# Kernel optimization log

Hardware: AMD Instinct MI355X
Metric: run time of the kernel (lower is better)

Reference implementation:

```python
import jax, jax.numpy as jnp
import numpy as np

B, L, D_IN = 4, 2048, 80
D, H, DFF, WIN = 128, 16, 128, 64
DH = D // H
BN_EPS = 1e-5


def sinusoidal_positional_encoding(l, d, dtype):
    # Faithful to source: pos_j = 10000 ** (j / d) (exponent j/d, not 2j/d)
    n = d // 2 + (d % 2 == 1)
    pos_i = jnp.arange(l, dtype=dtype)[:, None]                  # [L,1]
    pos_j = jnp.power(jnp.asarray(10000.0, dtype), jnp.arange(n, dtype=dtype) / d)  # [n]
    ang = pos_i / pos_j                                          # [L,n]
    pos = jnp.stack([jnp.sin(ang), jnp.cos(ang)], axis=-1).reshape(l, -1)
    return pos[:, :d]                                            # [L,D]


def local_window_disallowed_mask(l, win):
    # Source: mask starts as ones (True = disallowed), zeros only strictly
    i = jnp.arange(l)
    diff = jnp.abs(i[:, None] - i[None, :])
    allowed = (diff >= 1) & (diff <= win)
    return ~allowed                                              # [L,L] bool, True = masked


def setup_inputs() -> dict:
    key = jax.random.key(0)
    ks = jax.random.split(key, 17)
    s = 0.05  # weight scale for numerical stability
    return {
        "x": jax.random.normal(ks[0], (B, L, D_IN), jnp.float32),
        "conv_w": jax.random.normal(ks[1], (D, D_IN), jnp.float32) * s,
        "conv_b": jax.random.normal(ks[2], (D,), jnp.float32) * s,
        "bn_g": jax.random.uniform(ks[3], (D,), jnp.float32, 0.5, 1.5),
        "bn_b": jax.random.normal(ks[4], (D,), jnp.float32) * s,
        "bn_rm": jax.random.normal(ks[5], (D,), jnp.float32) * s,
        "bn_rv": jax.random.uniform(ks[6], (D,), jnp.float32, 0.5, 1.5),
        "in_proj_w": jax.random.normal(ks[7], (3 * D, D), jnp.float32) * s,
        "in_proj_b": jax.random.normal(ks[8], (3 * D,), jnp.float32) * s,
        "out_w": jax.random.normal(ks[9], (D, D), jnp.float32) * s,
        "out_b": jax.random.normal(ks[10], (D,), jnp.float32) * s,
        "ff_w1": jax.random.normal(ks[11], (DFF, D), jnp.float32) * s,
        "ff_b1": jax.random.normal(ks[12], (DFF,), jnp.float32) * s,
        "ff_w2": jax.random.normal(ks[13], (D, DFF), jnp.float32) * s,
        "ff_b2": jax.random.normal(ks[14], (D,), jnp.float32) * s,
        "fc_w": jax.random.normal(ks[15], (D_IN, D), jnp.float32) * s,
        "fc_b": jax.random.normal(ks[16], (D_IN,), jnp.float32) * s,
    }


def _forward(x, conv_w, conv_b, bn_g, bn_b, bn_rm, bn_rv,
             in_proj_w, in_proj_b, out_w, out_b,
             ff_w1, ff_b1, ff_w2, ff_b2, fc_w, fc_b):
    b, l, _ = x.shape
    dt = x.dtype
    # Conv1d(kernel=1) + ReLU + BatchNorm1d (eval mode, running stats)
    h = jax.nn.relu(jnp.einsum('bli,oi->blo', x, conv_w) + conv_b)     # [B,L,D]
    h = (h - bn_rm) * (bn_g * jax.lax.rsqrt(bn_rv + BN_EPS)) + bn_b
    # positional encoding
    h = h + sinusoidal_positional_encoding(l, D, dt)
    # MultiheadAttention (torch semantics: joint in_proj, scaled dot, out_proj)
    qkv = jnp.einsum('bld,ed->ble', h, in_proj_w) + in_proj_b          # [B,L,3D]
    q, k, v = jnp.split(qkv, 3, axis=-1)
    q = q.reshape(b, l, H, DH).transpose(0, 2, 1, 3)                   # [B,H,L,dh]
    k = k.reshape(b, l, H, DH).transpose(0, 2, 1, 3)
    v = v.reshape(b, l, H, DH).transpose(0, 2, 1, 3)
    scores = jnp.einsum('bhqd,bhkd->bhqk', q, k) / jnp.sqrt(jnp.asarray(DH, dt))
    mask = local_window_disallowed_mask(l, WIN)                        # True = masked
    scores = jnp.where(mask, jnp.finfo(dt).min, scores)
    attn = jax.nn.softmax(scores, axis=-1)                             # [B,H,L,L]
    ctx = jnp.einsum('bhqk,bhkd->bhqd', attn, v)
    ctx = ctx.transpose(0, 2, 1, 3).reshape(b, l, D)
    attn_out = jnp.einsum('bld,od->blo', ctx, out_w) + out_b           # [B,L,D]
    # FFN (no residual in source)
    f = jax.nn.relu(jnp.einsum('bld,fd->blf', attn_out, ff_w1) + ff_b1)
    f = jnp.einsum('blf,df->bld', f, ff_w2) + ff_b2                    # [B,L,D]
    # final head
    return jnp.einsum('bld,od->blo', f, fc_w) + fc_b                   # [B,L,80]


def reference(x, conv_w, conv_b, bn_g, bn_b, bn_rm, bn_rv,
              in_proj_w, in_proj_b, out_w, out_b,
              ff_w1, ff_b1, ff_w2, ff_b2, fc_w, fc_b):
    return _forward(x, conv_w, conv_b, bn_g, bn_b, bn_rm, bn_rv,
                    in_proj_w, in_proj_b, out_w, out_b,
                    ff_w1, ff_b1, ff_w2, ff_b2, fc_w, fc_b)
```

## Files before the change

### kernel.cpp

```cpp
#include <hip/hip_runtime.h>
#include <math.h>

constexpr int L_ = 2048, D_ = 128, H_ = 16;
constexpr int T_ = 8192;
constexpr int DIN = 80;
constexpr int LDX = T_;

typedef __attribute__((ext_vector_type(8))) short short8;
typedef __attribute__((ext_vector_type(4))) float floatx4;

__device__ float g_xT  [DIN * T_];
__device__ float g_posT[D_ * L_];
__device__ unsigned short g_h_hi[T_ * D_];
__device__ unsigned short g_h_lo[T_ * D_];
__device__ unsigned short g_Wq_hi[3 * D_ * D_];
__device__ unsigned short g_Wq_lo[3 * D_ * D_];
__device__ float g_qkv [3 * D_ * T_];
__device__ unsigned short g_ctxH[T_ * D_];
__device__ unsigned short g_ctxL[T_ * D_];
__device__ unsigned short g_Mf1H[D_ * D_];
__device__ unsigned short g_Mf1L[D_ * D_];
__device__ unsigned short g_MfcH[D_ * D_];
__device__ unsigned short g_MfcL[D_ * D_];
__device__ float g_WconvT[DIN * D_];
__device__ float g_bf1   [D_];
__device__ float g_bfc   [D_];

__device__ __forceinline__ unsigned short bf16h(float x) {
    unsigned u = __float_as_uint(x);
    return (unsigned short)((u + 0x7FFFu + ((u >> 16) & 1u)) >> 16);
}
__device__ __forceinline__ float bf16f(unsigned short h) {
    return __uint_as_float(((unsigned)h) << 16);
}

__global__ __launch_bounds__(256) void prep_kernel(
        const float* __restrict__ x,
        const float* __restrict__ conv_w,
        const float* __restrict__ in_proj_w,
        const float* __restrict__ out_w,  const float* __restrict__ out_b,
        const float* __restrict__ ff_w1,  const float* __restrict__ ff_b1,
        const float* __restrict__ ff_w2,  const float* __restrict__ ff_b2,
        const float* __restrict__ fc_w,   const float* __restrict__ fc_b) {
    __shared__ float smem[80 * 65];
    int bid = blockIdx.x, tid = threadIdx.x;

    if (bid < 128) {
        int t0 = bid * 64;
        for (int i = tid; i < 64 * 80; i += 256) {
            int t = i / 80, k = i - t * 80;
            smem[k * 65 + t] = x[(size_t)t0 * 80 + i];
        }
        __syncthreads();
        for (int i = tid; i < 80 * 64; i += 256) {
            int k = i >> 6, tt = i & 63;
            g_xT[(size_t)k * T_ + t0 + tt] = smem[k * 65 + tt];
        }
        return;
    }
    if (bid < 640) {
        int idx = (bid - 128) * 256 + tid;
        int l = idx >> 6, j = idx & 63;
        float inv = __expf((float)j * (-9.210340371976184f / 128.0f));
        float ang = (float)l * inv;
        g_posT[(2 * j) * L_ + l]     = sinf(ang);
        g_posT[(2 * j + 1) * L_ + l] = cosf(ang);
        return;
    }
    if (bid < 680) {
        int e = (bid - 640) * 256 + tid;
        int o = e / 80, k = e - o * 80;
        g_WconvT[k * D_ + o] = conv_w[e];
        return;
    }
    if (bid < 872) {
        int e = (bid - 680) * 256 + tid;
        float v = in_proj_w[e];
        unsigned short hi = bf16h(v);
        g_Wq_hi[e] = hi;
        g_Wq_lo[e] = bf16h(v - bf16f(hi));
        return;
    }
    float* rowbuf = smem;
    float* red = smem + 256;
    if (bid < 936) {
        int sub = tid >> 7, k = tid & 127;
        int f = (bid - 872) * 2 + sub;
        rowbuf[sub * 128 + k] = ff_w1[f * 128 + k];
        __syncthreads();
        float acc = 0.f;
#pragma unroll 8
        for (int o = 0; o < 128; o++)
            acc = fmaf(rowbuf[sub * 128 + o], out_w[o * 128 + k], acc);
        unsigned short hi = bf16h(acc);
        g_Mf1H[f * 128 + k] = hi;
        g_Mf1L[f * 128 + k] = bf16h(acc - bf16f(hi));
        red[tid] = rowbuf[sub * 128 + k] * out_b[k];
        __syncthreads();
        for (int s = 64; s > 0; s >>= 1) {
            if (k < s) red[tid] += red[tid + s];
            __syncthreads();
        }
        if (k == 0) g_bf1[f] = red[sub * 128] + ff_b1[f];
        return;
    }
    {
        int sub = tid >> 7, k = tid & 127;
        int o = (bid - 936) * 2 + sub;
        rowbuf[sub * 128 + k] = (o < 80) ? fc_w[o * 128 + k] : 0.f;
        __syncthreads();
        float acc = 0.f;
#pragma unroll 8
        for (int d = 0; d < 128; d++)
            acc = fmaf(rowbuf[sub * 128 + d], ff_w2[d * 128 + k], acc);
        unsigned short hi = bf16h(acc);
        g_MfcH[o * 128 + k] = hi;
        g_MfcL[o * 128 + k] = bf16h(acc - bf16f(hi));
        red[tid] = rowbuf[sub * 128 + k] * ff_b2[k];
        __syncthreads();
        for (int s = 64; s > 0; s >>= 1) {
            if (k < s) red[tid] += red[tid + s];
            __syncthreads();
        }
        if (k == 0) g_bfc[o] = (o < 80) ? (red[sub * 128] + fc_b[o]) : 0.f;
        return;
    }
}

__global__ __launch_bounds__(256) void conv_kernel(
        const float* __restrict__ X, const float* __restrict__ Wt,
        const float* __restrict__ bias,
        const float* __restrict__ bg, const float* __restrict__ bb,
        const float* __restrict__ brm, const float* __restrict__ brv) {
    constexpr int BK = 80, BN = 32, TN = 2;
    __shared__ float Xs[BK][64];
    __shared__ float Ws[BK][BN];
    int tid = threadIdx.x;
    int t0 = blockIdx.x * 64;
    int cb = blockIdx.y * BN;
    int tc = tid & 15, tr = tid >> 4;

    float acc[4][TN] = {};
    for (int i = tid; i < BK * 16; i += 256) {
        int k = i >> 4, f = i & 15;
        *(float4*)&Xs[k][f * 4] =
            *(const float4*)&X[(size_t)k * LDX + t0 + f * 4];
    }
    for (int i = tid; i < BK * (BN / 4); i += 256) {
        int k = i / (BN / 4), f = i - k * (BN / 4);
        *(float4*)&Ws[k][f * 4] =
            *(const float4*)&Wt[(size_t)k * D_ + cb + f * 4];
    }
    __syncthreads();
#pragma unroll 4
    for (int k = 0; k < BK; ++k) {
        float4 a = *(float4*)&Xs[k][tr * 4];
        float av[4] = {a.x, a.y, a.z, a.w};
        float wv[TN];
#pragma unroll
        for (int jj = 0; jj < TN; jj++) wv[jj] = Ws[k][tc * TN + jj];
#pragma unroll
        for (int i = 0; i < 4; i++)
#pragma unroll
            for (int jj = 0; jj < TN; jj++)
                acc[i][jj] = fmaf(av[i], wv[jj], acc[i][jj]);
    }

#pragma unroll
    for (int i = 0; i < 4; i++) {
        int t = t0 + tr * 4 + i;
        unsigned hi2 = 0, lo2 = 0;
#pragma unroll
        for (int jj = 0; jj < TN; jj++) {
            int c = cb + tc * TN + jj;
            float v = acc[i][jj] + bias[c];
            v = fmaxf(v, 0.0f);
            v = (v - brm[c]) * (bg[c] * rsqrtf(brv[c] + 1e-5f)) + bb[c];
            v += g_posT[c * L_ + (t & 2047)];
            unsigned short h = bf16h(v);
            float lo = v - bf16f(h);
            hi2 |= ((unsigned)h) << (16 * jj);
            lo2 |= ((unsigned)bf16h(lo)) << (16 * jj);
        }
        int cbase = cb + tc * TN;
        *(unsigned*)&g_h_hi[(size_t)t * 128 + cbase] = hi2;
        *(unsigned*)&g_h_lo[(size_t)t * 128 + cbase] = lo2;
    }
}

__global__ __launch_bounds__(256) void qkv_mfma(const float* __restrict__ in_proj_b) {
    __shared__ unsigned short WsH[64 * 136];
    __shared__ unsigned short WsL[64 * 136];
    __shared__ unsigned short HsH[32 * 136];
    __shared__ unsigned short HsL[32 * 136];
    int tid = threadIdx.x;
    int t0 = blockIdx.x * 32;
    int cb = blockIdx.y * 64;

    for (int i = tid; i < 1024; i += 256) {
        int r = i >> 4, c8 = (i & 15) * 8;
        *(uint4*)&WsH[r * 136 + c8] = *(const uint4*)&g_Wq_hi[(size_t)(cb + r) * 128 + c8];
        *(uint4*)&WsL[r * 136 + c8] = *(const uint4*)&g_Wq_lo[(size_t)(cb + r) * 128 + c8];
    }
    for (int i = tid; i < 512; i += 256) {
        int r = i >> 4, c8 = (i & 15) * 8;
        *(uint4*)&HsH[r * 136 + c8] = *(const uint4*)&g_h_hi[(size_t)(t0 + r) * 128 + c8];
        *(uint4*)&HsL[r * 136 + c8] = *(const uint4*)&g_h_lo[(size_t)(t0 + r) * 128 + c8];
    }
    __syncthreads();

    int lane = tid & 63, w = tid >> 6;
    int m16 = lane & 15, quad = lane >> 4;
    int c0 = w * 16;

    short8 aH[4], aL[4];
#pragma unroll
    for (int kt = 0; kt < 4; kt++) {
        aH[kt] = *(short8*)&WsH[(c0 + m16) * 136 + kt * 32 + quad * 8];
        aL[kt] = *(short8*)&WsL[(c0 + m16) * 136 + kt * 32 + quad * 8];
    }
    float bias_r[4];
#pragma unroll
    for (int r = 0; r < 4; r++) bias_r[r] = in_proj_b[cb + c0 + quad * 4 + r];

#pragma unroll
    for (int s = 0; s < 2; s++) {
        floatx4 acc = {0.f, 0.f, 0.f, 0.f};
        int trow = s * 16 + m16;
#pragma unroll
        for (int kt = 0; kt < 4; kt++) {
            short8 bH = *(short8*)&HsH[trow * 136 + kt * 32 + quad * 8];
            short8 bL = *(short8*)&HsL[trow * 136 + kt * 32 + quad * 8];
            acc = __builtin_amdgcn_mfma_f32_16x16x32_bf16(aH[kt], bH, acc, 0, 0, 0);
            acc = __builtin_amdgcn_mfma_f32_16x16x32_bf16(aL[kt], bH, acc, 0, 0, 0);
            acc = __builtin_amdgcn_mfma_f32_16x16x32_bf16(aH[kt], bL, acc, 0, 0, 0);
        }
#pragma unroll
        for (int r = 0; r < 4; r++)
            g_qkv[(size_t)(cb + c0 + quad * 4 + r) * LDX + t0 + s * 16 + m16] =
                acc[r] + bias_r[r];
    }
}

__global__ __launch_bounds__(256) void attn_kernel() {
    __shared__ float4 SK[2][2][324];
    __shared__ float4 SV[2][2][324];
    int bh = blockIdx.x;
    int qb = blockIdx.y * 512;
    int b = bh >> 4, h = bh & 15;
    int tb = b * L_;
    int tid = threadIdx.x;
    int jbase = qb - 64;

    for (int c16 = 0; c16 < 16; c16++) {
        int d = c16 & 7;
        int ch = ((c16 < 8) ? D_ : 2 * D_) + h * 8 + d;
        const float* src = g_qkv + (size_t)ch * LDX + tb;
        float4* base4 = ((c16 < 8) ? &SK[0][0][0] : &SV[0][0][0]) + (d >> 2) * 324;
        for (int s = tid; s < 641; s += 256) {
            int j = jbase + s;
            float v = ((unsigned)j < (unsigned)L_) ? src[j] : 0.f;
            ((float*)(base4 + (s & 1) * 648 + (s >> 1)))[d & 3] = v;
        }
    }
    __syncthreads();

    const float sc = 0.35355339059327373f;
    int q0 = qb + 2 * tid;
    float qa[8], qc[8];
#pragma unroll
    for (int d = 0; d < 8; d++) {
        qa[d] = g_qkv[(size_t)(h * 8 + d) * LDX + tb + q0] * sc;
        qc[d] = g_qkv[(size_t)(h * 8 + d) * LDX + tb + q0 + 1] * sc;
    }
    float l0 = 0.f, l1 = 0.f;
    float A0[8] = {}, A1[8] = {};
    int j00 = jbase + 2 * tid;

#pragma unroll 2
    for (int it = 0; it <= 129; it++) {
        int pp = it & 1, idx = tid + (it >> 1);
        float4 ka = SK[pp][0][idx], kb2 = SK[pp][1][idx];
        float kv[8] = {ka.x, ka.y, ka.z, ka.w, kb2.x, kb2.y, kb2.z, kb2.w};
        float s0 = 0.f, s1 = 0.f;
#pragma unroll
        for (int d = 0; d < 8; d++) {
            s0 = fmaf(qa[d], kv[d], s0);
            s1 = fmaf(qc[d], kv[d], s1);
        }
        bool jv = (unsigned)(j00 + it) < (unsigned)L_;
        float w0 = (jv && it != 64 && it <= 128) ? __expf(s0) : 0.f;
        float w1 = (jv && it != 65 && it >= 1)  ? __expf(s1) : 0.f;
        l0 += w0; l1 += w1;
        float4 va = SV[pp][0][idx], vb2 = SV[pp][1][idx];
        float vv[8] = {va.x, va.y, va.z, va.w, vb2.x, vb2.y, vb2.z, vb2.w};
#pragma unroll
        for (int d = 0; d < 8; d++) {
            A0[d] = fmaf(w0, vv[d], A0[d]);
            A1[d] = fmaf(w1, vv[d], A1[d]);
        }
    }
    float i0 = 1.f / l0, i1 = 1.f / l1;
    unsigned hp[4], lp[4];
#pragma unroll
    for (int d2 = 0; d2 < 4; d2++) {
        float v0 = A0[2 * d2] * i0, v1 = A0[2 * d2 + 1] * i0;
        unsigned short h0 = bf16h(v0), h1 = bf16h(v1);
        hp[d2] = (unsigned)h0 | ((unsigned)h1 << 16);
        lp[d2] = (unsigned)bf16h(v0 - bf16f(h0)) |
                 ((unsigned)bf16h(v1 - bf16f(h1)) << 16);
    }
    *(uint4*)&g_ctxH[(size_t)(tb + q0) * 128 + h * 8] = *(uint4*)hp;
    *(uint4*)&g_ctxL[(size_t)(tb + q0) * 128 + h * 8] = *(uint4*)lp;
#pragma unroll
    for (int d2 = 0; d2 < 4; d2++) {
        float v0 = A1[2 * d2] * i1, v1 = A1[2 * d2 + 1] * i1;
        unsigned short h0 = bf16h(v0), h1 = bf16h(v1);
        hp[d2] = (unsigned)h0 | ((unsigned)h1 << 16);
        lp[d2] = (unsigned)bf16h(v0 - bf16f(h0)) |
                 ((unsigned)bf16h(v1 - bf16f(h1)) << 16);
    }
    *(uint4*)&g_ctxH[(size_t)(tb + q0 + 1) * 128 + h * 8] = *(uint4*)hp;
    *(uint4*)&g_ctxL[(size_t)(tb + q0 + 1) * 128 + h * 8] = *(uint4*)lp;
}

__global__ __launch_bounds__(256) void f1fc_mfma(float* __restrict__ out) {
    __shared__ unsigned short sm[4 * 32 * 136];
    unsigned short* ctxH = sm;
    unsigned short* ctxL = sm + 32 * 136;
    unsigned short* C1H  = sm + 2 * 32 * 136;
    unsigned short* C1L  = sm + 3 * 32 * 136;
    float* C2 = (float*)sm;
    __shared__ float b1s[128];

    int tid = threadIdx.x;
    int t0 = blockIdx.x * 32;

    for (int i = tid; i < 512; i += 256) {
        int r = i >> 4, c8 = (i & 15) * 8;
        *(uint4*)&ctxH[r * 136 + c8] = *(const uint4*)&g_ctxH[(size_t)(t0 + r) * 128 + c8];
        *(uint4*)&ctxL[r * 136 + c8] = *(const uint4*)&g_ctxL[(size_t)(t0 + r) * 128 + c8];
    }
    if (tid < 128) b1s[tid] = g_bf1[tid];
    __syncthreads();

    int lane = tid & 63, w = tid >> 6;
    int m16 = lane & 15, quad = lane >> 4;

    floatx4 acc1[2][2];
#pragma unroll
    for (int mt = 0; mt < 2; mt++) {
        int fbase = w * 32 + mt * 16 + m16;
        short8 aH[4], aL[4];
#pragma unroll
        for (int kt = 0; kt < 4; kt++) {
            aH[kt] = *(const short8*)&g_Mf1H[(size_t)fbase * 128 + kt * 32 + quad * 8];
            aL[kt] = *(const short8*)&g_Mf1L[(size_t)fbase * 128 + kt * 32 + quad * 8];
        }
#pragma unroll
        for (int nt = 0; nt < 2; nt++) {
            floatx4 acc = {0.f, 0.f, 0.f, 0.f};
            int trow = nt * 16 + m16;
#pragma unroll
            for (int kt = 0; kt < 4; kt++) {
                short8 bH = *(short8*)&ctxH[trow * 136 + kt * 32 + quad * 8];
                short8 bL = *(short8*)&ctxL[trow * 136 + kt * 32 + quad * 8];
                acc = __builtin_amdgcn_mfma_f32_16x16x32_bf16(aH[kt], bH, acc, 0, 0, 0);
                acc = __builtin_amdgcn_mfma_f32_16x16x32_bf16(aL[kt], bH, acc, 0, 0, 0);
                acc = __builtin_amdgcn_mfma_f32_16x16x32_bf16(aH[kt], bL, acc, 0, 0, 0);
            }
            acc1[mt][nt] = acc;
        }
    }
#pragma unroll
    for (int mt = 0; mt < 2; mt++) {
#pragma unroll
        for (int nt = 0; nt < 2; nt++) {
            int f0 = w * 32 + mt * 16 + quad * 4;
            int t = nt * 16 + m16;
            float v[4];
#pragma unroll
            for (int r = 0; r < 4; r++)
                v[r] = fmaxf(acc1[mt][nt][r] + b1s[f0 + r], 0.f);
            unsigned short h0 = bf16h(v[0]), h1 = bf16h(v[1]);
            unsigned short h2 = bf16h(v[2]), h3 = bf16h(v[3]);
            *(unsigned*)&C1H[t * 136 + f0]     = (unsigned)h0 | ((unsigned)h1 << 16);
            *(unsigned*)&C1H[t * 136 + f0 + 2] = (unsigned)h2 | ((unsigned)h3 << 16);
            *(unsigned*)&C1L[t * 136 + f0] =
                (unsigned)bf16h(v[0] - bf16f(h0)) | ((unsigned)bf16h(v[1] - bf16f(h1)) << 16);
            *(unsigned*)&C1L[t * 136 + f0 + 2] =
                (unsigned)bf16h(v[2] - bf16f(h2)) | ((unsigned)bf16h(v[3] - bf16f(h3)) << 16);
        }
    }
    __syncthreads();

    floatx4 acc2[2][2];
#pragma unroll
    for (int mt = 0; mt < 2; mt++) {
        int obase = w * 32 + mt * 16 + m16;
        short8 aH[4], aL[4];
#pragma unroll
        for (int kt = 0; kt < 4; kt++) {
            aH[kt] = *(const short8*)&g_MfcH[(size_t)obase * 128 + kt * 32 + quad * 8];
            aL[kt] = *(const short8*)&g_MfcL[(size_t)obase * 128 + kt * 32 + quad * 8];
        }
#pragma unroll
        for (int nt = 0; nt < 2; nt++) {
            floatx4 acc = {0.f, 0.f, 0.f, 0.f};
            int trow = nt * 16 + m16;
#pragma unroll
            for (int kt = 0; kt < 4; kt++) {
                short8 bH = *(short8*)&C1H[trow * 136 + kt * 32 + quad * 8];
                short8 bL = *(short8*)&C1L[trow * 136 + kt * 32 + quad * 8];
                acc = __builtin_amdgcn_mfma_f32_16x16x32_bf16(aH[kt], bH, acc, 0, 0, 0);
                acc = __builtin_amdgcn_mfma_f32_16x16x32_bf16(aL[kt], bH, acc, 0, 0, 0);
                acc = __builtin_amdgcn_mfma_f32_16x16x32_bf16(aH[kt], bL, acc, 0, 0, 0);
            }
            acc2[mt][nt] = acc;
        }
    }
    __syncthreads();
#pragma unroll
    for (int mt = 0; mt < 2; mt++) {
        int o0 = w * 32 + mt * 16 + quad * 4;
        if (o0 < 96) {
#pragma unroll
            for (int nt = 0; nt < 2; nt++) {
                int t = nt * 16 + m16;
#pragma unroll
                for (int r = 0; r < 4; r++)
                    C2[t * 100 + o0 + r] = acc2[mt][nt][r] + g_bfc[o0 + r];
            }
        }
    }
    __syncthreads();
    for (int i = tid; i < 640; i += 256) {
        int t = i / 20, c4 = i - t * 20;
        *(float4*)&out[(size_t)(t0 + t) * 80 + c4 * 4] = *(float4*)&C2[t * 100 + c4 * 4];
    }
}

extern "C" void kernel_launch(void* const* d_in, const int* in_sizes, int n_in,
                              void* d_out, int out_size, void* d_ws, size_t ws_size,
                              hipStream_t stream) {
    const float* x         = (const float*)d_in[0];
    const float* conv_w    = (const float*)d_in[1];
    const float* conv_b    = (const float*)d_in[2];
    const float* bn_g      = (const float*)d_in[3];
    const float* bn_b      = (const float*)d_in[4];
    const float* bn_rm     = (const float*)d_in[5];
    const float* bn_rv     = (const float*)d_in[6];
    const float* in_proj_w = (const float*)d_in[7];
    const float* in_proj_b = (const float*)d_in[8];
    const float* out_w     = (const float*)d_in[9];
    const float* out_b     = (const float*)d_in[10];
    const float* ff_w1     = (const float*)d_in[11];
    const float* ff_b1     = (const float*)d_in[12];
    const float* ff_w2     = (const float*)d_in[13];
    const float* ff_b2     = (const float*)d_in[14];
    const float* fc_w      = (const float*)d_in[15];
    const float* fc_b      = (const float*)d_in[16];

    float *p_xT, *p_WconvT;
    hipGetSymbolAddress((void**)&p_xT,     HIP_SYMBOL(g_xT));
    hipGetSymbolAddress((void**)&p_WconvT, HIP_SYMBOL(g_WconvT));

    prep_kernel<<<1000, 256, 0, stream>>>(x, conv_w, in_proj_w, out_w, out_b,
                                          ff_w1, ff_b1, ff_w2, ff_b2, fc_w, fc_b);

    conv_kernel<<<dim3(128, 4), 256, 0, stream>>>(
        p_xT, p_WconvT, conv_b, bn_g, bn_b, bn_rm, bn_rv);

    qkv_mfma<<<dim3(256, 6), 256, 0, stream>>>(in_proj_b);

    attn_kernel<<<dim3(64, 4), 256, 0, stream>>>();

    f1fc_mfma<<<256, 256, 0, stream>>>((float*)d_out);
}
```

Before: 154.7 us.

## Fuse input prep and conv into one stage with bf16x3 MFMA

Merges the prep kernel and the conv kernel into a single stage1 kernel. The 1x1 conv now runs on bf16 MFMA using a hi/lo split (three products), and the positional encoding is computed inline instead of through a precomputed table. The x transpose buffer, the transposed conv weights and the posT table are removed, which saves one launch and several global round-trips. In exchange, sin/cos is evaluated per output element, and the split-bf16 precision differs slightly from the fp32 FMA conv it replaces.

After: 146.7 us. -5.2%, faster.

```diff
diff --git a/kernel.cpp b/kernel.cpp
--- a/kernel.cpp
+++ b/kernel.cpp
@@ -3,14 +3,11 @@
 
 constexpr int L_ = 2048, D_ = 128, H_ = 16;
 constexpr int T_ = 8192;
-constexpr int DIN = 80;
 constexpr int LDX = T_;
 
 typedef __attribute__((ext_vector_type(8))) short short8;
 typedef __attribute__((ext_vector_type(4))) float floatx4;
 
-__device__ float g_xT  [DIN * T_];
-__device__ float g_posT[D_ * L_];
 __device__ unsigned short g_h_hi[T_ * D_];
 __device__ unsigned short g_h_lo[T_ * D_];
 __device__ unsigned short g_Wq_hi[3 * D_ * D_];
@@ -22,9 +19,8 @@
 __device__ unsigned short g_Mf1L[D_ * D_];
 __device__ unsigned short g_MfcH[D_ * D_];
 __device__ unsigned short g_MfcL[D_ * D_];
-__device__ float g_WconvT[DIN * D_];
-__device__ float g_bf1   [D_];
-__device__ float g_bfc   [D_];
+__device__ float g_bf1 [D_];
+__device__ float g_bfc [D_];
 
 __device__ __forceinline__ unsigned short bf16h(float x) {
     unsigned u = __float_as_uint(x);
@@ -34,58 +30,133 @@
     return __uint_as_float(((unsigned)h) << 16);
 }
 
-__global__ __launch_bounds__(256) void prep_kernel(
-        const float* __restrict__ x,
-        const float* __restrict__ conv_w,
+__global__ __launch_bounds__(256) void stage1_kernel(
+        const float* __restrict__ x, const float* __restrict__ conv_w,
+        const float* __restrict__ conv_b,
+        const float* __restrict__ bg, const float* __restrict__ bb,
+        const float* __restrict__ brm, const float* __restrict__ brv,
         const float* __restrict__ in_proj_w,
         const float* __restrict__ out_w,  const float* __restrict__ out_b,
         const float* __restrict__ ff_w1,  const float* __restrict__ ff_b1,
         const float* __restrict__ ff_w2,  const float* __restrict__ ff_b2,
         const float* __restrict__ fc_w,   const float* __restrict__ fc_b) {
-    __shared__ float smem[80 * 65];
+    __shared__ unsigned short sm[2 * 32 * 104];
     int bid = blockIdx.x, tid = threadIdx.x;
 
-    if (bid < 128) {
-        int t0 = bid * 64;
-        for (int i = tid; i < 64 * 80; i += 256) {
-            int t = i / 80, k = i - t * 80;
-            smem[k * 65 + t] = x[(size_t)t0 * 80 + i];
+    if (bid < 256) {
+        unsigned short* XsH = sm;
+        unsigned short* XsL = sm + 32 * 104;
+        int t0 = bid * 32;
+
+        for (int p = tid; p < 1280; p += 256) {
+            int f0 = p * 2;
+            int r = f0 / 80, k = f0 - r * 80;
+            float2 v2 = *(const float2*)&x[(size_t)(t0 + r) * 80 + k];
+            unsigned short h0 = bf16h(v2.x), h1 = bf16h(v2.y);
+            *(unsigned*)&XsH[r * 104 + k] = (unsigned)h0 | ((unsigned)h1 << 16);
+            *(unsigned*)&XsL[r * 104 + k] =
+                (unsigned)bf16h(v2.x - bf16f(h0)) |
+                ((unsigned)bf16h(v2.y - bf16f(h1)) << 16);
+        }
+        for (int i = tid; i < 384; i += 256) {
+            int r = i / 12, k = 80 + 2 * (i - r * 12);
+            *(unsigned*)&XsH[r * 104 + k] = 0u;
+            *(unsigned*)&XsL[r * 104 + k] = 0u;
         }
         __syncthreads();
-        for (int i = tid; i < 80 * 64; i += 256) {
-            int k = i >> 6, tt = i & 63;
-            g_xT[(size_t)k * T_ + t0 + tt] = smem[k * 65 + tt];
+
+        int lane = tid & 63, w = tid >> 6;
+        int m16 = lane & 15, quad = lane >> 4;
+
+        short8 aH[2][3], aL[2][3];
+#pragma unroll
+        for (int mt = 0; mt < 2; mt++) {
+            int c = w * 32 + mt * 16 + m16;
+#pragma unroll
+            for (int kt = 0; kt < 3; kt++) {
+                int kb = kt * 32 + quad * 8;
+                short8 vh = {0, 0, 0, 0, 0, 0, 0, 0};
+                short8 vl = {0, 0, 0, 0, 0, 0, 0, 0};
+                if (kb < 80) {
+                    float4 f0 = *(const float4*)&conv_w[(size_t)c * 80 + kb];
+                    float4 f1 = *(const float4*)&conv_w[(size_t)c * 80 + kb + 4];
+                    float vv[8] = {f0.x, f0.y, f0.z, f0.w, f1.x, f1.y, f1.z, f1.w};
+#pragma unroll
+                    for (int e = 0; e < 8; e++) {
+                        unsigned short hh = bf16h(vv[e]);
+                        vh[e] = (short)hh;
+                        vl[e] = (short)bf16h(vv[e] - bf16f(hh));
+                    }
+                }
+                aH[mt][kt] = vh; aL[mt][kt] = vl;
+            }
+        }
+
+#pragma unroll
+        for (int mt = 0; mt < 2; mt++) {
+#pragma unroll
+            for (int nt = 0; nt < 2; nt++) {
+                floatx4 acc = {0.f, 0.f, 0.f, 0.f};
+                int trow = nt * 16 + m16;
+#pragma unroll
+                for (int kt = 0; kt < 3; kt++) {
+                    short8 bHv = *(short8*)&XsH[trow * 104 + kt * 32 + quad * 8];
+                    short8 bLv = *(short8*)&XsL[trow * 104 + kt * 32 + quad * 8];
+                    acc = __builtin_amdgcn_mfma_f32_16x16x32_bf16(aH[mt][kt], bHv, acc, 0, 0, 0);
+                    acc = __builtin_amdgcn_mfma_f32_16x16x32_bf16(aL[mt][kt], bHv, acc, 0, 0, 0);
+                    acc = __builtin_amdgcn_mfma_f32_16x16x32_bf16(aH[mt][kt], bLv, acc, 0, 0, 0);
+                }
+                int c0 = w * 32 + mt * 16 + quad * 4;
+                int t = t0 + nt * 16 + m16;
+                int l = t & 2047;
+                float vr[4];
+#pragma unroll
+                for (int r = 0; r < 4; r++) {
+                    int c = c0 + r;
+                    float v = acc[r] + conv_b[c];
+                    v = fmaxf(v, 0.0f);
+                    v = (v - brm[c]) * (bg[c] * rsqrtf(brv[c] + 1e-5f)) + bb[c];
+                    float inv = __expf((float)(c >> 1) * (-9.210340371976184f / 128.0f));
+                    float ang = (float)l * inv;
+                    v += (c & 1) ? cosf(ang) : sinf(ang);
+                    vr[r] = v;
+                }
+                unsigned short h0 = bf16h(vr[0]), h1 = bf16h(vr[1]);
+                unsigned short h2 = bf16h(vr[2]), h3 = bf16h(vr[3]);
+                unsigned hp[2] = {(unsigned)h0 | ((unsigned)h1 << 16),
+                                  (unsigned)h2 | ((unsigned)h3 << 16)};
+                unsigned lp[2] = {
+                    (unsigned)bf16h(vr[0] - bf16f(h0)) | ((unsigned)bf16h(vr[1] - bf16f(h1)) << 16),
+                    (unsigned)bf16h(vr[2] - bf16f(h2)) | ((unsigned)bf16h(vr[3] - bf16f(h3)) << 16)};
+                *(uint2*)&g_h_hi[(size_t)t * 128 + c0] = *(uint2*)hp;
+                *(uint2*)&g_h_lo[(size_t)t * 128 + c0] = *(uint2*)lp;
+            }
         }
         return;
     }
-    if (bid < 640) {
-        int idx = (bid - 128) * 256 + tid;
-        int l = idx >> 6, j = idx & 63;
-        float inv = __expf((float)j * (-9.210340371976184f / 128.0f));
-        float ang = (float)l * inv;
-        g_posT[(2 * j) * L_ + l]     = sinf(ang);
-        g_posT[(2 * j + 1) * L_ + l] = cosf(ang);
+    if (bid < 304) {
+        int e4 = ((bid - 256) * 256 + tid) * 4;
+        float4 v = *(const float4*)&in_proj_w[e4];
+        float vv[4] = {v.x, v.y, v.z, v.w};
+        unsigned short hh[4], ll[4];
+#pragma unroll
+        for (int e = 0; e < 4; e++) {
+            hh[e] = bf16h(vv[e]);
+            ll[e] = bf16h(vv[e] - bf16f(hh[e]));
+        }
+        unsigned hp[2] = {(unsigned)hh[0] | ((unsigned)hh[1] << 16),
+                          (unsigned)hh[2] | ((unsigned)hh[3] << 16)};
+        unsigned lp[2] = {(unsigned)ll[0] | ((unsigned)ll[1] << 16),
+                          (unsigned)ll[2] | ((unsigned)ll[3] << 16)};
+        *(uint2*)&g_Wq_hi[e4] = *(uint2*)hp;
+        *(uint2*)&g_Wq_lo[e4] = *(uint2*)lp;
         return;
     }
-    if (bid < 680) {
-        int e = (bid - 640) * 256 + tid;
-        int o = e / 80, k = e - o * 80;
-        g_WconvT[k * D_ + o] = conv_w[e];
-        return;
-    }
-    if (bid < 872) {
-        int e = (bid - 680) * 256 + tid;
-        float v = in_proj_w[e];
-        unsigned short hi = bf16h(v);
-        g_Wq_hi[e] = hi;
-        g_Wq_lo[e] = bf16h(v - bf16f(hi));
-        return;
-    }
-    float* rowbuf = smem;
-    float* red = smem + 256;
-    if (bid < 936) {
+    float* rowbuf = (float*)sm;
+    float* red = (float*)sm + 256;
+    if (bid < 368) {
         int sub = tid >> 7, k = tid & 127;
-        int f = (bid - 872) * 2 + sub;
+        int f = (bid - 304) * 2 + sub;
         rowbuf[sub * 128 + k] = ff_w1[f * 128 + k];
         __syncthreads();
         float acc = 0.f;
@@ -106,7 +177,7 @@
     }
     {
         int sub = tid >> 7, k = tid & 127;
-        int o = (bid - 936) * 2 + sub;
+        int o = (bid - 368) * 2 + sub;
         rowbuf[sub * 128 + k] = (o < 80) ? fc_w[o * 128 + k] : 0.f;
         __syncthreads();
         float acc = 0.f;
@@ -124,67 +195,6 @@
         }
         if (k == 0) g_bfc[o] = (o < 80) ? (red[sub * 128] + fc_b[o]) : 0.f;
         return;
-    }
-}
-
-__global__ __launch_bounds__(256) void conv_kernel(
-        const float* __restrict__ X, const float* __restrict__ Wt,
-        const float* __restrict__ bias,
-        const float* __restrict__ bg, const float* __restrict__ bb,
-        const float* __restrict__ brm, const float* __restrict__ brv) {
-    constexpr int BK = 80, BN = 32, TN = 2;
-    __shared__ float Xs[BK][64];
-    __shared__ float Ws[BK][BN];
-    int tid = threadIdx.x;
-    int t0 = blockIdx.x * 64;
-    int cb = blockIdx.y * BN;
-    int tc = tid & 15, tr = tid >> 4;
-
-    float acc[4][TN] = {};
-    for (int i = tid; i < BK * 16; i += 256) {
-        int k = i >> 4, f = i & 15;
-        *(float4*)&Xs[k][f * 4] =
-            *(const float4*)&X[(size_t)k * LDX + t0 + f * 4];
-    }
-    for (int i = tid; i < BK * (BN / 4); i += 256) {
-        int k = i / (BN / 4), f = i - k * (BN / 4);
-        *(float4*)&Ws[k][f * 4] =
-            *(const float4*)&Wt[(size_t)k * D_ + cb + f * 4];
-    }
-    __syncthreads();
-#pragma unroll 4
-    for (int k = 0; k < BK; ++k) {
-        float4 a = *(float4*)&Xs[k][tr * 4];
-        float av[4] = {a.x, a.y, a.z, a.w};
-        float wv[TN];
-#pragma unroll
-        for (int jj = 0; jj < TN; jj++) wv[jj] = Ws[k][tc * TN + jj];
-#pragma unroll
-        for (int i = 0; i < 4; i++)
-#pragma unroll
-            for (int jj = 0; jj < TN; jj++)
-                acc[i][jj] = fmaf(av[i], wv[jj], acc[i][jj]);
-    }
-
-#pragma unroll
-    for (int i = 0; i < 4; i++) {
-        int t = t0 + tr * 4 + i;
-        unsigned hi2 = 0, lo2 = 0;
-#pragma unroll
-        for (int jj = 0; jj < TN; jj++) {
-            int c = cb + tc * TN + jj;
-            float v = acc[i][jj] + bias[c];
-            v = fmaxf(v, 0.0f);
-            v = (v - brm[c]) * (bg[c] * rsqrtf(brv[c] + 1e-5f)) + bb[c];
-            v += g_posT[c * L_ + (t & 2047)];
-            unsigned short h = bf16h(v);
-            float lo = v - bf16f(h);
-            hi2 |= ((unsigned)h) << (16 * jj);
-            lo2 |= ((unsigned)bf16h(lo)) << (16 * jj);
-        }
-        int cbase = cb + tc * TN;
-        *(unsigned*)&g_h_hi[(size_t)t * 128 + cbase] = hi2;
-        *(unsigned*)&g_h_lo[(size_t)t * 128 + cbase] = lo2;
     }
 }
 
@@ -461,15 +471,10 @@
     const float* fc_w      = (const float*)d_in[15];
     const float* fc_b      = (const float*)d_in[16];
 
-    float *p_xT, *p_WconvT;
-    hipGetSymbolAddress((void**)&p_xT,     HIP_SYMBOL(g_xT));
-    hipGetSymbolAddress((void**)&p_WconvT, HIP_SYMBOL(g_WconvT));
-
-    prep_kernel<<<1000, 256, 0, stream>>>(x, conv_w, in_proj_w, out_w, out_b,
-                                          ff_w1, ff_b1, ff_w2, ff_b2, fc_w, fc_b);
-
-    conv_kernel<<<dim3(128, 4), 256, 0, stream>>>(
-        p_xT, p_WconvT, conv_b, bn_g, bn_b, bn_rm, bn_rv);
+    stage1_kernel<<<432, 256, 0, stream>>>(x, conv_w, conv_b, bn_g, bn_b,
+                                           bn_rm, bn_rv, in_proj_w,
+                                           out_w, out_b, ff_w1, ff_b1,
+                                           ff_w2, ff_b2, fc_w, fc_b);
 
     qkv_mfma<<<dim3(256, 6), 256, 0, stream>>>(in_proj_b);
 
```
